# Performance work log

Measured on AMD Instinct MI355X. Metric: run time of the kernel, lower is better.

## Reference

```python
import jax, jax.numpy as jnp
import numpy as np
from jax import lax

GS = 29          # grid_size
DW = 15          # displacement_width
DR = 0.4         # disp_range
N = GS ** 3      # 24389 control points
P = DW ** 2      # 225 in-plane displacements
WIN = (1, 1, 3, 3, 1)
ONE = (1, 1, 1, 1, 1)


def _axis(n):
    # align_corners=False pixel-center coords in [-1, 1], as torch affine_grid
    return (2.0 * jnp.arange(n, dtype=jnp.float32) + 1.0) / n - 1.0


def make_grids():
    a = _axis(GS)
    zc, yc, xc = jnp.meshgrid(a, a, a, indexing='ij')
    grid_xyz = jnp.stack([xc, yc, zc], -1).reshape(-1, 3)  # (N,3) xyz, d-major flatten
    s = DR * _axis(DW)
    A, B = jnp.meshgrid(s, s, indexing='ij')
    Z = jnp.zeros_like(A)
    sx = jnp.stack([B, A, Z], -1).reshape(-1, 3)  # z=0 plane: (s[w], s[h], 0)
    sy = jnp.stack([B, Z, A], -1).reshape(-1, 3)  # y=0 plane: (s[w], 0, s[d])
    sz = jnp.stack([Z, B, A], -1).reshape(-1, 3)  # x=0 plane: (0, s[h], s[d])
    shift_2d = jnp.stack([sx, sy, sz], axis=1)    # (P,3,3): [disp, plane, xyz]
    return grid_xyz, shift_2d


def trilerp(vol, coords, border):
    # vol (C,D,H,W); coords (...,3) normalized xyz; align_corners=False trilinear
    C, D, H, W = vol.shape
    vflat = vol.reshape(C, -1)
    x, y, z = coords[..., 0], coords[..., 1], coords[..., 2]
    ix = 0.5 * ((x + 1.0) * W - 1.0)
    iy = 0.5 * ((y + 1.0) * H - 1.0)
    iz = 0.5 * ((z + 1.0) * D - 1.0)
    x0 = jnp.floor(ix); y0 = jnp.floor(iy); z0 = jnp.floor(iz)
    fx, fy, fz = ix - x0, iy - y0, iz - z0
    x0 = x0.astype(jnp.int32); y0 = y0.astype(jnp.int32); z0 = z0.astype(jnp.int32)
    out = 0.0
    for dz in (0, 1):
        wz = fz if dz else 1.0 - fz
        zi = z0 + dz
        for dy in (0, 1):
            wy = fy if dy else 1.0 - fy
            yi = y0 + dy
            for dx in (0, 1):
                wx = fx if dx else 1.0 - fx
                xi = x0 + dx
                w = wx * wy * wz
                xc = jnp.clip(xi, 0, W - 1)
                yc = jnp.clip(yi, 0, H - 1)
                zc = jnp.clip(zi, 0, D - 1)
                if not border:  # padding_mode='zeros'
                    inb = ((xi >= 0) & (xi < W) & (yi >= 0) & (yi < H) & (zi >= 0) & (zi < D))
                    w = w * inb.astype(vol.dtype)
                idx = (zc * H + yc) * W + xc
                out = out + vflat[:, idx] * w
    return out  # (C, *coords.shape[:-1])


def pad_dh(x):
    # ReplicationPad3d((0,0,2,2,2,2)) on a 5D tensor: pad dims 2 and 3 by 2
    return jnp.pad(x, ((0, 0), (0, 0), (2, 2), (2, 2), (0, 0)), mode='edge')


def minpool(x):
    # -MaxPool3d((3,3,1))(-x)
    return -lax.reduce_window(-x, -jnp.inf, lax.max, WIN, ONE, 'VALID')


def avgpool(x):
    # AvgPool3d((3,3,1), stride=1)
    return lax.reduce_window(x, 0.0, lax.add, WIN, ONE, 'VALID') / 9.0


def grid_smooth(cost):
    # (1,N,DW,DW,3) -> two 3x3 avg passes over the 29^3 control grid (d,h axes)
    cp = cost.transpose(2, 3, 4, 0, 1).reshape(1, 3 * P, GS, GS, GS)
    cp = avgpool(avgpool(pad_dh(cp)))
    return cp.transpose(0, 2, 3, 4, 1).reshape(1, N, DW, DW, 3)


def setup_inputs() -> dict:
    key = jax.random.key(0)
    k1, k2 = jax.random.split(key)
    C, V = 8, 64
    feat00 = jax.random.normal(k1, (1, C, V, V, V), jnp.float32)
    feat50 = jax.random.normal(k2, (1, C, V, V, V), jnp.float32)
    grid_xyz, shift_2d = make_grids()
    shift_2d_min = jnp.array(jnp.broadcast_to(shift_2d[None, None], (1, N, P, 3, 3)))
    alpha = jnp.array([1.0, 0.1, 1.0, 1.0, 0.1, 5.0], jnp.float32)
    return {"feat00": feat00, "feat50": feat50, "shift_2d_min": shift_2d_min,
            "grid_xyz": grid_xyz, "shift_2d": shift_2d, "alpha": alpha}


def reference(feat00, feat50, shift_2d_min, grid_xyz, shift_2d, alpha):
    grid29 = grid_xyz.reshape(GS, GS * GS, 3)
    sm = shift_2d_min.reshape(GS, GS * GS, P, 3, 3)
    f00, f50 = feat00[0], feat50[0]

    def chunk(args):
        g, s = args                                                # (841,3), (841,P,3,3)
        mov = trilerp(f50, g[:, None, None, :] + s, border=True)   # (C,841,P,3)
        fix = trilerp(f00, g, border=False)                        # (C,841)
        ssd = jnp.sum((fix[:, :, None, None] - mov) ** 2, axis=0)  # (841,P,3)
        return alpha[1] + alpha[0] * ssd

    pdd = lax.map(chunk, (grid29, sm)).reshape(1, N, DW, DW, 3)
    cost = avgpool(minpool(pad_dh(pdd)))
    cost = alpha[4] + alpha[2] * pdd + alpha[3] * grid_smooth(cost)
    cost = avgpool(minpool(pad_dh(cost)))
    cost_avg = grid_smooth(cost).reshape(N, P, 3)
    cost_soft = jax.nn.softmax(-alpha[5] * cost_avg, axis=1)
    pred_xyz = 0.5 * jnp.einsum('npk,pkd->nd', cost_soft, shift_2d)
    return cost_soft.reshape(N, 1, DW, DW, 3), pred_xyz, cost_avg
```

## Files before the change

### kernel.cpp

```cpp
#include <hip/hip_runtime.h>
#include <math.h>

#define GS   29
#define GS2  841
#define NCP  24389
#define DW   15
#define PP   225
#define CH   675
#define CHP  676
#define CC   8
#define VV   64
#define V3   262144

typedef __attribute__((ext_vector_type(8))) _Float16 half8;
typedef __attribute__((ext_vector_type(4))) _Float16 half4;

__device__ __forceinline__ float sv(int i) {
    return 0.4f * ((2.f * i + 1.f) * (1.f / 15.f) - 1.f);
}

__global__ __launch_bounds__(256) void make_vols(const float* __restrict__ in,
                                                 _Float16* __restrict__ volA,
                                                 _Float16* __restrict__ volB) {
    int v = blockIdx.x * 256 + threadIdx.x;
    if (v >= V3) return;
    int z = v >> 12, y = (v >> 6) & 63, x = v & 63;
    half8 h;
#pragma unroll
    for (int c = 0; c < CC; c++) h[c] = (_Float16)in[c * V3 + v];
    *(half8*)(volA + (size_t)v * 8) = h;
    *(half8*)(volB + (size_t)((((z << 6) | x) << 6) | y) * 8) = h;
}

__global__ __launch_bounds__(256) void pdd_pool_n(const float* __restrict__ f00,
                                                  const _Float16* __restrict__ volA,
                                                  const _Float16* __restrict__ volB,
                                                  const float* __restrict__ grid,
                                                  const float* __restrict__ alpha,
                                                  _Float16* __restrict__ pdd,
                                                  _Float16* __restrict__ pool) {
    int n = blockIdx.x;
    int tid = threadIdx.x;
    __shared__ __align__(16) _Float16 fixh[8];
    __shared__ float rowp[CH];
    __shared__ float smin[3 * 289];

    float gx = grid[n * 3 + 0], gy = grid[n * 3 + 1], gz = grid[n * 3 + 2];

    if (tid < 8) {
        float ix = 0.5f * ((gx + 1.f) * VV - 1.f);
        float iy = 0.5f * ((gy + 1.f) * VV - 1.f);
        float iz = 0.5f * ((gz + 1.f) * VV - 1.f);
        float x0f = floorf(ix), y0f = floorf(iy), z0f = floorf(iz);
        float fx = ix - x0f, fy = iy - y0f, fz = iz - z0f;
        int x0 = (int)x0f, y0 = (int)y0f, z0 = (int)z0f;
        const float* fc = f00 + tid * V3;
        float acc = 0.f;
        for (int dz = 0; dz < 2; dz++) {
            int zi = z0 + dz; float wz = dz ? fz : 1.f - fz;
            for (int dy = 0; dy < 2; dy++) {
                int yi = y0 + dy; float wy = dy ? fy : 1.f - fy;
                for (int dx = 0; dx < 2; dx++) {
                    int xi = x0 + dx; float wx = dx ? fx : 1.f - fx;
                    if (xi >= 0 && xi < VV && yi >= 0 && yi < VV && zi >= 0 && zi < VV)
                        acc += wx * wy * wz * fc[(zi * VV + yi) * VV + xi];
                }
            }
        }
        fixh[tid] = (_Float16)acc;
    }
    __syncthreads();

    if (tid < PP) {
        int p = tid;
        int h_ = p / 15, w_ = p - 15 * h_;
        float A = sv(h_), B = sv(w_);
        half8 f8 = *(const half8*)fixh;
        float a0 = alpha[0], a1 = alpha[1];

        for (int k = 0; k < 3; k++) {
            float pu, pv, pw;
            const _Float16* vol;
            if (k == 0)      { pu = gx + B; pv = gy + A; pw = gz;     vol = volA; }
            else if (k == 1) { pu = gx + B; pv = gy;     pw = gz + A; vol = volA; }
            else             { pu = gy + B; pv = gx;     pw = gz + A; vol = volB; }

            float iu = 0.5f * ((pu + 1.f) * VV - 1.f);
            float iv = 0.5f * ((pv + 1.f) * VV - 1.f);
            float iw = 0.5f * ((pw + 1.f) * VV - 1.f);
            float u0f = floorf(iu), v0f = floorf(iv), w0f = floorf(iw);
            float fu = iu - u0f, fv = iv - v0f, fw = iw - w0f;
            int u0 = (int)u0f, v0 = (int)v0f, w0 = (int)w0f;

            int p0 = min(max(u0, 0), VV - 2);
            float wAu = (u0 < 0) ? 1.f : ((u0 >= VV - 1) ? 0.f : (1.f - fu));
            float wBu = 1.f - wAu;
            int v0c = min(max(v0, 0), VV - 1), v1c = min(max(v0 + 1, 0), VV - 1);
            int w0c = min(max(w0, 0), VV - 1), w1c = min(max(w0 + 1, 0), VV - 1);
            float wv0 = 1.f - fv, wv1 = fv;
            float ww0 = 1.f - fw, ww1 = fw;

            half8 acc = {0, 0, 0, 0, 0, 0, 0, 0};
#define PAIR(WC, VC, WGT) {                                               \
                float fA_ = (WGT) * wAu, fB_ = (WGT) * wBu;               \
                _Float16 hA_ = (_Float16)fA_, hB_ = (_Float16)fB_;        \
                half8 hA8 = {hA_, hA_, hA_, hA_, hA_, hA_, hA_, hA_};     \
                half8 hB8 = {hB_, hB_, hB_, hB_, hB_, hB_, hB_, hB_};     \
                const _Float16* vp = vol + (size_t)((((WC) * VV) + (VC)) * VV + p0) * 8; \
                half8 lo = *(const half8*)vp;                             \
                half8 hi = *(const half8*)(vp + 8);                       \
                acc += hA8 * lo;                                          \
                acc += hB8 * hi;                                          \
            }
            PAIR(w0c, v0c, ww0 * wv0)
            PAIR(w0c, v1c, ww0 * wv1)
            PAIR(w1c, v0c, ww1 * wv0)
            PAIR(w1c, v1c, ww1 * wv1)
#undef PAIR

            half8 d8 = f8 - acc;
            float ssd = 0.f;
#pragma unroll
            for (int c = 0; c < 8; c++) { float dc = (float)d8[c]; ssd = fmaf(dc, dc, ssd); }
            rowp[p * 3 + k] = a1 + a0 * ssd;
        }
    }
    __syncthreads();

    for (int idx = tid; idx < 867; idx += 256) {
        int k = idx / 289; int r = idx - 289 * k; int a = r / 17; int b = r - 17 * a;
        float mn = 1e30f;
        for (int u = 0; u < 3; u++) {
            int hh = min(max(a + u - 2, 0), 14);
            for (int v = 0; v < 3; v++) {
                int ww = min(max(b + v - 2, 0), 14);
                mn = fminf(mn, rowp[(hh * 15 + ww) * 3 + k]);
            }
        }
        smin[idx] = mn;
    }
    __syncthreads();

    for (int i = tid; i < CH; i += 256) {
        pdd[(size_t)n * CHP + i] = (_Float16)rowp[i];
        int p = i / 3, k = i - 3 * p;
        int h = p / 15, w = p - 15 * h;
        float acc = 0.f;
        for (int a = 0; a < 3; a++)
            for (int b = 0; b < 3; b++)
                acc += smin[k * 289 + (h + a) * 17 + (w + b)];
        pool[(size_t)n * CHP + i] = (_Float16)(acc * (1.f / 9.f));
    }
}

__global__ __launch_bounds__(256) void cost_pool2(const _Float16* __restrict__ pool1,
                                                  const _Float16* __restrict__ pdd,
                                                  const float* __restrict__ alpha,
                                                  _Float16* __restrict__ pool2) {
    int n = blockIdx.x, tid = threadIdx.x;
    int x = n % GS; int zy = n / GS; int y = zy % GS; int z = zy / GS;
    __shared__ int   sbase[25];
    __shared__ float swt[25];
    __shared__ float rowp[CHP];
    __shared__ float smn[17 * 17 * 3];

    if (tid < 25) {
        int dz = tid / 5, dy = tid - 5 * (tid / 5);
        int zz = min(max(z + dz - 2, 0), GS - 1);
        int yy = min(max(y + dy - 2, 0), GS - 1);
        sbase[tid] = ((zz * GS + yy) * GS + x) * CHP;
        float tz = 3.f - fabsf((float)dz - 2.f);
        float ty = 3.f - fabsf((float)dy - 2.f);
        swt[tid] = tz * ty * (1.f / 81.f);
    }
    __syncthreads();

    if (tid < 169) {
        int c0 = tid * 4;
        float s0 = 0.f, s1 = 0.f, s2 = 0.f, s3 = 0.f;
#pragma unroll
        for (int t = 0; t < 25; t++) {
            int off = sbase[t] + c0;
            float w = swt[t];
            half4 hv = *(const half4*)(pool1 + off);
            s0 = fmaf(w, (float)hv[0], s0);
            s1 = fmaf(w, (float)hv[1], s1);
            s2 = fmaf(w, (float)hv[2], s2);
            s3 = fmaf(w, (float)hv[3], s3);
        }
        float a2 = alpha[2], a3 = alpha[3], a4 = alpha[4];
        half4 pv = *(const half4*)(pdd + (size_t)n * CHP + c0);
        rowp[c0 + 0] = a4 + a2 * (float)pv[0] + a3 * s0;
        rowp[c0 + 1] = a4 + a2 * (float)pv[1] + a3 * s1;
        rowp[c0 + 2] = a4 + a2 * (float)pv[2] + a3 * s2;
        rowp[c0 + 3] = a4 + a2 * (float)pv[3] + a3 * s3;
    }
    __syncthreads();

    for (int idx = tid; idx < 867; idx += 256) {
        int k = idx / 289; int r = idx - 289 * k; int a = r / 17; int b = r - 17 * a;
        float mn = 1e30f;
        for (int u = 0; u < 3; u++) {
            int hh = min(max(a + u - 2, 0), 14);
            for (int v = 0; v < 3; v++) {
                int ww = min(max(b + v - 2, 0), 14);
                mn = fminf(mn, rowp[(hh * 15 + ww) * 3 + k]);
            }
        }
        smn[idx] = mn;
    }
    __syncthreads();

    for (int i = tid; i < CH; i += 256) {
        int p = i / 3, k = i - 3 * p;
        int h = p / 15, w = p - 15 * h;
        float acc = 0.f;
        for (int a = 0; a < 3; a++)
            for (int b = 0; b < 3; b++)
                acc += smn[k * 289 + (h + a) * 17 + (w + b)];
        pool2[(size_t)n * CHP + i] = (_Float16)(acc * (1.f / 9.f));
    }
}

__global__ __launch_bounds__(256) void smooth_softmax(const _Float16* __restrict__ pool2,
                                                      const float* __restrict__ alpha,
                                                      float* __restrict__ ca,
                                                      float* __restrict__ soft,
                                                      float* __restrict__ pred) {
    int n = blockIdx.x, tid = threadIdx.x;
    int x = n % GS; int zy = n / GS; int y = zy % GS; int z = zy / GS;
    int wave = tid >> 6, lane = tid & 63;
    __shared__ int   sbase[25];
    __shared__ float swt[25];
    __shared__ float vals[CHP];
    __shared__ float partial[3][3];

    if (tid < 25) {
        int dz = tid / 5, dy = tid - 5 * (tid / 5);
        int zz = min(max(z + dz - 2, 0), GS - 1);
        int yy = min(max(y + dy - 2, 0), GS - 1);
        sbase[tid] = ((zz * GS + yy) * GS + x) * CHP;
        float tz = 3.f - fabsf((float)dz - 2.f);
        float ty = 3.f - fabsf((float)dy - 2.f);
        swt[tid] = tz * ty * (1.f / 81.f);
    }
    __syncthreads();

    if (tid < 169) {
        int c0 = tid * 4;
        float s0 = 0.f, s1 = 0.f, s2 = 0.f, s3 = 0.f;
#pragma unroll
        for (int t = 0; t < 25; t++) {
            int off = sbase[t] + c0;
            float w = swt[t];
            half4 hv = *(const half4*)(pool2 + off);
            s0 = fmaf(w, (float)hv[0], s0);
            s1 = fmaf(w, (float)hv[1], s1);
            s2 = fmaf(w, (float)hv[2], s2);
            s3 = fmaf(w, (float)hv[3], s3);
        }
        vals[c0 + 0] = s0;
        vals[c0 + 1] = s1;
        vals[c0 + 2] = s2;
        vals[c0 + 3] = s3;
    }
    __syncthreads();

    for (int i = tid; i < CH; i += 256) ca[(size_t)n * CH + i] = vals[i];
    __syncthreads();

    float a5 = alpha[5];
    if (wave < 3) {
        int k = wave;
        float v[4], e[4];
        float m = -1e30f;
#pragma unroll
        for (int j = 0; j < 4; j++) {
            int p = lane + 64 * j;
            v[j] = (p < PP) ? -a5 * vals[p * 3 + k] : -1e30f;
            m = fmaxf(m, v[j]);
        }
#pragma unroll
        for (int o = 32; o > 0; o >>= 1) m = fmaxf(m, __shfl_xor(m, o));
        float sum = 0.f;
#pragma unroll
        for (int j = 0; j < 4; j++) {
            int p = lane + 64 * j;
            e[j] = (p < PP) ? __expf(v[j] - m) : 0.f;
            sum += e[j];
        }
#pragma unroll
        for (int o = 32; o > 0; o >>= 1) sum += __shfl_xor(sum, o);
        float inv = 1.f / sum;
        float px = 0.f, py = 0.f, pz = 0.f;
#pragma unroll
        for (int j = 0; j < 4; j++) {
            int p = lane + 64 * j;
            if (p < PP) {
                float s = e[j] * inv;
                vals[p * 3 + k] = s;
                int h_ = p / 15, w_ = p - 15 * h_;
                float A = sv(h_), B = sv(w_);
                if (k == 0)      { px += s * B; py += s * A; }
                else if (k == 1) { px += s * B; pz += s * A; }
                else             { py += s * B; pz += s * A; }
            }
        }
#pragma unroll
        for (int o = 32; o > 0; o >>= 1) {
            px += __shfl_xor(px, o);
            py += __shfl_xor(py, o);
            pz += __shfl_xor(pz, o);
        }
        if (lane == 0) { partial[k][0] = px; partial[k][1] = py; partial[k][2] = pz; }
    }
    __syncthreads();
    if (tid < 3) pred[(size_t)n * 3 + tid] = 0.5f * (partial[0][tid] + partial[1][tid] + partial[2][tid]);
    for (int i = tid; i < CH; i += 256) soft[(size_t)n * CH + i] = vals[i];
}

extern "C" void kernel_launch(void* const* d_in, const int* in_sizes, int n_in,
                              void* d_out, int out_size, void* d_ws, size_t ws_size,
                              hipStream_t stream) {
    const float* f00   = (const float*)d_in[0];
    const float* f50   = (const float*)d_in[1];
    const float* grid  = (const float*)d_in[3];
    const float* alpha = (const float*)d_in[5];

    float* out0 = (float*)d_out;
    float* out1 = out0 + (size_t)NCP * CH;
    float* out2 = out1 + (size_t)NCP * 3;

    char* ws = (char*)d_ws;
    _Float16* volA = (_Float16*)ws;
    _Float16* volB = volA + (size_t)V3 * 8;
    _Float16* H0 = volB + (size_t)V3 * 8;
    _Float16* H1 = H0 + (size_t)NCP * CHP;
    _Float16* H2 = H1 + (size_t)NCP * CHP;

    make_vols<<<(V3 + 255) / 256, 256, 0, stream>>>(f50, volA, volB);

    pdd_pool_n<<<NCP, 256, 0, stream>>>(f00, volA, volB, grid, alpha, H0, H1);

    cost_pool2<<<NCP, 256, 0, stream>>>(H1, H0, alpha, H2);

    smooth_softmax<<<NCP, 256, 0, stream>>>(H2, alpha, out2, out0, out1);
}
```

Baseline: 572.5 us.

## Split 5x5 grid smoothing into separable z-pass kernel and y-pass

Replaces the 25-tap 2D (z,y) triangular smoothing gather in cost_pool2 and smooth_softmax with a separable scheme: a new gs_z4 kernel does a sliding-window 5-tap z pass per column, and the downstream kernels do only a 5-tap y pass. This cuts global reads per output from 25 to about 5+1, reducing memory traffic in the two heavy kernels. It adds two extra kernel launches and an extra intermediate write/read of the full fp16 cost volume, and reuses H1 as the output buffer of the first y pass.

After: 534.2 us. 1.07x faster.

```diff
diff --git a/kernel.cpp b/kernel.cpp
--- a/kernel.cpp
+++ b/kernel.cpp
@@ -153,36 +153,59 @@
     }
 }
 
-__global__ __launch_bounds__(256) void cost_pool2(const _Float16* __restrict__ pool1,
-                                                  const _Float16* __restrict__ pdd,
-                                                  const float* __restrict__ alpha,
-                                                  _Float16* __restrict__ pool2) {
+__global__ __launch_bounds__(256) void gs_z4(const _Float16* __restrict__ in,
+                                             _Float16* __restrict__ out) {
+    const int COLS = GS2 * 169;
+    int id = blockIdx.x * 256 + threadIdx.x;
+    if (id >= COLS) return;
+    int row = id / 169, c4 = id - 169 * row;
+    size_t base = (size_t)row * CHP + c4 * 4;
+    const size_t ZS = (size_t)GS2 * CHP;
+    const float w0 = 1.f / 9.f, w1 = 2.f / 9.f, w2 = 3.f / 9.f;
+
+    half4 h0 = *(const half4*)(in + base);
+    half4 h3 = *(const half4*)(in + base + ZS);
+    half4 h4 = *(const half4*)(in + base + 2 * ZS);
+    float v0[4], v1[4], v2[4], v3[4], v4[4];
+#pragma unroll
+    for (int j = 0; j < 4; j++) {
+        v0[j] = (float)h0[j]; v1[j] = v0[j]; v2[j] = v0[j];
+        v3[j] = (float)h3[j]; v4[j] = (float)h4[j];
+    }
+    for (int z = 0; z < GS; z++) {
+        half4 o;
+#pragma unroll
+        for (int j = 0; j < 4; j++)
+            o[j] = (_Float16)(w0 * (v0[j] + v4[j]) + w1 * (v1[j] + v3[j]) + w2 * v2[j]);
+        *(half4*)(out + base + (size_t)z * ZS) = o;
+        int zn = z + 3; if (zn > GS - 1) zn = GS - 1;
+        half4 hn = *(const half4*)(in + base + (size_t)zn * ZS);
+#pragma unroll
+        for (int j = 0; j < 4; j++) {
+            v0[j] = v1[j]; v1[j] = v2[j]; v2[j] = v3[j]; v3[j] = v4[j];
+            v4[j] = (float)hn[j];
+        }
+    }
+}
+
+__global__ __launch_bounds__(256) void cost_pool2_y(const _Float16* __restrict__ zs,
+                                                    const _Float16* __restrict__ pdd,
+                                                    const float* __restrict__ alpha,
+                                                    _Float16* __restrict__ pool2) {
     int n = blockIdx.x, tid = threadIdx.x;
     int x = n % GS; int zy = n / GS; int y = zy % GS; int z = zy / GS;
-    __shared__ int   sbase[25];
-    __shared__ float swt[25];
     __shared__ float rowp[CHP];
     __shared__ float smn[17 * 17 * 3];
-
-    if (tid < 25) {
-        int dz = tid / 5, dy = tid - 5 * (tid / 5);
-        int zz = min(max(z + dz - 2, 0), GS - 1);
-        int yy = min(max(y + dy - 2, 0), GS - 1);
-        sbase[tid] = ((zz * GS + yy) * GS + x) * CHP;
-        float tz = 3.f - fabsf((float)dz - 2.f);
-        float ty = 3.f - fabsf((float)dy - 2.f);
-        swt[tid] = tz * ty * (1.f / 81.f);
-    }
-    __syncthreads();
 
     if (tid < 169) {
         int c0 = tid * 4;
         float s0 = 0.f, s1 = 0.f, s2 = 0.f, s3 = 0.f;
 #pragma unroll
-        for (int t = 0; t < 25; t++) {
-            int off = sbase[t] + c0;
-            float w = swt[t];
-            half4 hv = *(const half4*)(pool1 + off);
+        for (int dy = 0; dy < 5; dy++) {
+            int yy = min(max(y + dy - 2, 0), GS - 1);
+            size_t off = ((size_t)(z * GS + yy) * GS + x) * CHP + c0;
+            float w = (3.f - fabsf((float)dy - 2.f)) * (1.f / 9.f);
+            half4 hv = *(const half4*)(zs + off);
             s0 = fmaf(w, (float)hv[0], s0);
             s1 = fmaf(w, (float)hv[1], s1);
             s2 = fmaf(w, (float)hv[2], s2);
@@ -222,38 +245,26 @@
     }
 }
 
-__global__ __launch_bounds__(256) void smooth_softmax(const _Float16* __restrict__ pool2,
-                                                      const float* __restrict__ alpha,
-                                                      float* __restrict__ ca,
-                                                      float* __restrict__ soft,
-                                                      float* __restrict__ pred) {
+__global__ __launch_bounds__(256) void smooth_y_softmax(const _Float16* __restrict__ zs,
+                                                        const float* __restrict__ alpha,
+                                                        float* __restrict__ ca,
+                                                        float* __restrict__ soft,
+                                                        float* __restrict__ pred) {
     int n = blockIdx.x, tid = threadIdx.x;
     int x = n % GS; int zy = n / GS; int y = zy % GS; int z = zy / GS;
     int wave = tid >> 6, lane = tid & 63;
-    __shared__ int   sbase[25];
-    __shared__ float swt[25];
     __shared__ float vals[CHP];
     __shared__ float partial[3][3];
-
-    if (tid < 25) {
-        int dz = tid / 5, dy = tid - 5 * (tid / 5);
-        int zz = min(max(z + dz - 2, 0), GS - 1);
-        int yy = min(max(y + dy - 2, 0), GS - 1);
-        sbase[tid] = ((zz * GS + yy) * GS + x) * CHP;
-        float tz = 3.f - fabsf((float)dz - 2.f);
-        float ty = 3.f - fabsf((float)dy - 2.f);
-        swt[tid] = tz * ty * (1.f / 81.f);
-    }
-    __syncthreads();
 
     if (tid < 169) {
         int c0 = tid * 4;
         float s0 = 0.f, s1 = 0.f, s2 = 0.f, s3 = 0.f;
 #pragma unroll
-        for (int t = 0; t < 25; t++) {
-            int off = sbase[t] + c0;
-            float w = swt[t];
-            half4 hv = *(const half4*)(pool2 + off);
+        for (int dy = 0; dy < 5; dy++) {
+            int yy = min(max(y + dy - 2, 0), GS - 1);
+            size_t off = ((size_t)(z * GS + yy) * GS + x) * CHP + c0;
+            float w = (3.f - fabsf((float)dy - 2.f)) * (1.f / 9.f);
+            half4 hv = *(const half4*)(zs + off);
             s0 = fmaf(w, (float)hv[0], s0);
             s1 = fmaf(w, (float)hv[1], s1);
             s2 = fmaf(w, (float)hv[2], s2);
@@ -342,7 +353,12 @@
 
     pdd_pool_n<<<NCP, 256, 0, stream>>>(f00, volA, volB, grid, alpha, H0, H1);
 
-    cost_pool2<<<NCP, 256, 0, stream>>>(H1, H0, alpha, H2);
-
-    smooth_softmax<<<NCP, 256, 0, stream>>>(H2, alpha, out2, out0, out1);
-}
+    const int COLS = GS2 * 169;
+    const int gbz = (COLS + 255) / 256;
+
+    gs_z4<<<gbz, 256, 0, stream>>>(H1, H2);
+    cost_pool2_y<<<NCP, 256, 0, stream>>>(H2, H0, alpha, H1);
+
+    gs_z4<<<gbz, 256, 0, stream>>>(H1, H2);
+    smooth_y_softmax<<<NCP, 256, 0, stream>>>(H2, alpha, out2, out0, out1);
+}
```
